# Performance work log

Measured on AMD Instinct MI355X. Metric: run time of the kernel, lower is better.

Reference implementation:

```python
import jax, jax.numpy as jnp
import numpy as np

N = 50000
D_IN = 256
OUT = 16
HEADS = 32
GAT_C = OUT  # out_channels + beta_on(=0)


def _gat_conv(x, src, dst, W, att_src, att_dst, bias):
    """PyG GATConv, concat=False (mean over heads), with self-loops already appended."""
    n = x.shape[0]
    xp = (x @ W).reshape(n, HEADS, GAT_C)            # [N,H,C]
    a_s = jnp.einsum('nhc,hc->nh', xp, att_src)       # [N,H]
    a_d = jnp.einsum('nhc,hc->nh', xp, att_dst)       # [N,H]
    e = jax.nn.leaky_relu(a_s[src] + a_d[dst], 0.2)   # [E,H]
    # segment softmax over incoming edges of each dst node
    m = jax.ops.segment_max(e, dst, num_segments=n)
    e = jnp.exp(e - m[dst])
    s = jax.ops.segment_sum(e, dst, num_segments=n)
    alpha = e / (s[dst] + 1e-16)                      # [E,H]
    out = jax.ops.segment_sum(alpha[:, :, None] * xp[src], dst, num_segments=n)  # [N,H,C]
    return out.mean(axis=1) + bias                    # [N,C]


def setup_inputs() -> dict:
    key = jax.random.key(0)
    ks = jax.random.split(key, 16)
    E = 800000
    x = jax.random.normal(ks[0], (N, D_IN), dtype=jnp.float32)
    edge_index = jax.random.randint(ks[1], (2, E), 0, N, dtype=jnp.int64)
    sc = 1.0 / np.sqrt(D_IN)
    W1 = jax.random.normal(ks[2], (D_IN, HEADS * GAT_C), dtype=jnp.float32) * sc
    att_src1 = jax.random.normal(ks[3], (HEADS, GAT_C), dtype=jnp.float32) * 0.1
    att_dst1 = jax.random.normal(ks[4], (HEADS, GAT_C), dtype=jnp.float32) * 0.1
    b1 = jnp.zeros((GAT_C,), dtype=jnp.float32)
    W2 = jax.random.normal(ks[5], (D_IN, HEADS * GAT_C), dtype=jnp.float32) * sc
    att_src2 = jax.random.normal(ks[6], (HEADS, GAT_C), dtype=jnp.float32) * 0.1
    att_dst2 = jax.random.normal(ks[7], (HEADS, GAT_C), dtype=jnp.float32) * 0.1
    b2 = jnp.zeros((GAT_C,), dtype=jnp.float32)
    lin1_w = jax.random.normal(ks[8], (D_IN, 4 * OUT), dtype=jnp.float32) * sc
    lin1_b = jnp.zeros((4 * OUT,), dtype=jnp.float32)
    lin2_w = jax.random.normal(ks[9], (4 * OUT, OUT), dtype=jnp.float32) * (1.0 / np.sqrt(4 * OUT))
    lin2_b = jnp.zeros((OUT,), dtype=jnp.float32)
    return {"x": x, "edge_index": edge_index,
            "W1": W1, "att_src1": att_src1, "att_dst1": att_dst1, "b1": b1,
            "W2": W2, "att_src2": att_src2, "att_dst2": att_dst2, "b2": b2,
            "lin1_w": lin1_w, "lin1_b": lin1_b, "lin2_w": lin2_w, "lin2_b": lin2_b}


def reference(x, edge_index, W1, att_src1, att_dst1, b1, W2, att_src2, att_dst2, b2,
              lin1_w, lin1_b, lin2_w, lin2_b):
    n = x.shape[0]
    loops = jnp.arange(n, dtype=edge_index.dtype)
    # conv1: flow source_to_target on edge_index -> aggregate src=row0 into dst=row1
    src = jnp.concatenate([edge_index[0], loops])
    dst = jnp.concatenate([edge_index[1], loops])
    x_in = jax.nn.elu(_gat_conv(x, src, dst, W1, att_src1, att_dst1, b1))
    # conv2: flow target_to_source on transposed edge_index -> same effective (src,dst)
    x_out = jax.nn.elu(_gat_conv(x, src, dst, W2, att_src2, att_dst2, b2))
    x1 = jax.nn.elu(x @ lin1_w + lin1_b)
    x_self = jax.nn.elu(x1 @ lin2_w + lin2_b)
    return (x_in, x_out, x_self)
```

## Files before the change

### kernel.cpp

```cpp
#include <hip/hip_runtime.h>

typedef __bf16 bf16x8 __attribute__((ext_vector_type(8)));
typedef float  f32x4  __attribute__((ext_vector_type(4)));
typedef float  f32x2  __attribute__((ext_vector_type(2)));

#define NNODES   50000
#define DIN      256
#define HEADS    32
#define CDIM     16
#define NH       512
#define ERAW     800000
#define SCAN_B   196
#define LDSW     280

__device__ __forceinline__ float b2f(unsigned short u) {
    return __uint_as_float(((unsigned)u) << 16);
}
__device__ __forceinline__ unsigned short f2b(float f) {
    unsigned v = __float_as_uint(f);
    v += 0x7fffu + ((v >> 16) & 1u);
    return (unsigned short)(v >> 16);
}

__global__ void k_detect(const int* __restrict__ ei, int* __restrict__ flag) {
    if (threadIdx.x == 0 && blockIdx.x == 0) {
        int nz = 0;
        #pragma unroll
        for (int t = 0; t < 64; ++t) nz |= ei[2 * t + 1];
        flag[0] = (nz == 0) ? 1 : 0;
    }
}

__global__ void k_zero_deg(int* __restrict__ deg) {
    int i = blockIdx.x * 256 + threadIdx.x;
    if (i < NNODES) deg[i] = 0;
}

__global__ void k_hist(const int* __restrict__ ei, const int* __restrict__ flag,
                       int* __restrict__ deg) {
    int e = blockIdx.x * 256 + threadIdx.x;
    int d = flag[0] ? ei[2 * ERAW + 2 * e] : ei[ERAW + e];
    atomicAdd(&deg[d], 1);
}

__global__ void k_scan_blk(const int* __restrict__ deg, int* __restrict__ part,
                           int* __restrict__ bsum) {
    __shared__ int sm[256];
    int b = blockIdx.x, t = threadIdx.x, i = b * 256 + t;
    int v = (i < NNODES) ? deg[i] : 0;
    sm[t] = v; __syncthreads();
    for (int off = 1; off < 256; off <<= 1) {
        int u = (t >= off) ? sm[t - off] : 0;
        __syncthreads();
        sm[t] += u; __syncthreads();
    }
    if (i < NNODES) part[i] = sm[t] - v;
    if (t == 255) bsum[b] = sm[255];
}

__global__ void k_scan_top(int* __restrict__ bsum) {
    __shared__ int sm[256];
    int t = threadIdx.x;
    int v = (t < SCAN_B) ? bsum[t] : 0;
    sm[t] = v; __syncthreads();
    for (int off = 1; off < 256; off <<= 1) {
        int u = (t >= off) ? sm[t - off] : 0;
        __syncthreads();
        sm[t] += u; __syncthreads();
    }
    if (t < SCAN_B) bsum[t] = sm[t] - v;
}

__global__ void k_scan_add(const int* __restrict__ part, const int* __restrict__ bsum,
                           int* __restrict__ rs, int* __restrict__ cur) {
    int b = blockIdx.x, t = threadIdx.x, i = b * 256 + t;
    if (i < NNODES) { int r = part[i] + bsum[b]; rs[i] = r; cur[i] = r; }
}

__global__ void k_scatter(const int* __restrict__ ei, const int* __restrict__ flag,
                          int* __restrict__ cur, int* __restrict__ csr) {
    int e = blockIdx.x * 256 + threadIdx.x;
    int s, d;
    if (flag[0]) { s = ei[2 * e]; d = ei[2 * ERAW + 2 * e]; }
    else         { s = ei[e];     d = ei[ERAW + e]; }
    int pos = atomicAdd(&cur[d], 1);
    csr[pos] = s;
}

__global__ void k_cast_x(const float* __restrict__ x, unsigned short* __restrict__ xb) {
    int i = blockIdx.x * 256 + threadIdx.x;
    float4 v = *(const float4*)(x + (size_t)i * 4);
    ushort4 o;
    o.x = f2b(v.x); o.y = f2b(v.y); o.z = f2b(v.z); o.w = f2b(v.w);
    *(ushort4*)(xb + (size_t)i * 4) = o;
}

__global__ void k_tr(const float* __restrict__ src, unsigned short* __restrict__ dst,
                     int K, int N) {
    int n = blockIdx.x, k = threadIdx.x;
    dst[n * K + k] = f2b(src[k * N + n]);
}

__global__ void k_tr_gat(const float* __restrict__ src, unsigned short* __restrict__ dst) {
    int n = blockIdx.x, k = threadIdx.x;
    int p = (n & ~63) | (((n & 15) << 2) | ((n >> 4) & 3));
    dst[n * DIN + k] = f2b(src[k * NH + p]);
}

__global__ void __launch_bounds__(256)
k_gemm_xp(const unsigned short* __restrict__ xb,
          const unsigned short* __restrict__ Wt,
          unsigned* __restrict__ xp8) {
    __shared__ unsigned short As[64 * LDSW];
    int row0 = blockIdx.x * 64;
    int tid = threadIdx.x;
    int w = tid >> 6, lane = tid & 63;
    int r = lane & 15, quad = lane >> 4;

    {
        int row = tid >> 2, slot = tid & 3;
        const uint4* g = (const uint4*)(xb + (size_t)(row0 + row) * DIN);
        uint4* l = (uint4*)(As + row * LDSW);
        #pragma unroll
        for (int i = 0; i < 8; ++i)
            l[slot + 4 * i] = g[slot + 4 * i];
    }
    __syncthreads();

    #pragma unroll
    for (int ch = 0; ch < 2; ++ch) {
        f32x4 acc[4][4] = {};
        #pragma unroll
        for (int kc = 0; kc < 8; ++kc) {
            bf16x8 a[4], b[4];
            #pragma unroll
            for (int sub = 0; sub < 4; ++sub)
                a[sub] = *(const bf16x8*)(As + (sub * 16 + r) * LDSW + kc * 32 + quad * 8);
            #pragma unroll
            for (int t = 0; t < 4; ++t) {
                int col = ch * 256 + w * 64 + t * 16 + r;
                b[t] = *(const bf16x8*)(Wt + (size_t)col * DIN + kc * 32 + quad * 8);
            }
            #pragma unroll
            for (int t = 0; t < 4; ++t)
                #pragma unroll
                for (int sub = 0; sub < 4; ++sub)
                    acc[sub][t] = __builtin_amdgcn_mfma_f32_16x16x32_bf16(a[sub], b[t], acc[sub][t], 0, 0, 0);
        }
        #pragma unroll
        for (int sub = 0; sub < 4; ++sub) {
            #pragma unroll
            for (int j = 0; j < 4; ++j) {
                int row = row0 + sub * 16 + quad * 4 + j;
                if (row < NNODES) {
                    unsigned u = (unsigned)__builtin_amdgcn_cvt_pk_fp8_f32(
                                     acc[sub][0][j], acc[sub][1][j], 0, false);
                    u = (unsigned)__builtin_amdgcn_cvt_pk_fp8_f32(
                                     acc[sub][2][j], acc[sub][3][j], (int)u, true);
                    xp8[(size_t)row * 128 + ch * 64 + w * 16 + r] = u;
                }
            }
        }
    }
}

__global__ void k_att(const unsigned* __restrict__ xp8,
                      const float* __restrict__ att_src,
                      const float* __restrict__ att_dst,
                      float* __restrict__ a_s, float* __restrict__ a_d) {
    int tid = threadIdx.x;
    int nd = blockIdx.x * 4 + (tid >> 6);
    int ln = tid & 63;
    int h = ln >> 1;

    const uint2 q = *(const uint2*)(xp8 + (size_t)nd * 128 + ln * 2);
    f32x2 p0 = __builtin_amdgcn_cvt_pk_f32_fp8((int)q.x, false);
    f32x2 p1 = __builtin_amdgcn_cvt_pk_f32_fp8((int)q.x, true);
    f32x2 p2 = __builtin_amdgcn_cvt_pk_f32_fp8((int)q.y, false);
    f32x2 p3 = __builtin_amdgcn_cvt_pk_f32_fp8((int)q.y, true);
    float f[8] = {p0.x, p0.y, p1.x, p1.y, p2.x, p2.y, p3.x, p3.y};

    const f32x4* As4 = (const f32x4*)att_src;
    const f32x4* Ad4 = (const f32x4*)att_dst;
    f32x4 s0 = As4[ln * 2], s1 = As4[ln * 2 + 1];
    f32x4 d0 = Ad4[ln * 2], d1 = Ad4[ln * 2 + 1];

    float ps = f[0]*s0.x + f[1]*s0.y + f[2]*s0.z + f[3]*s0.w
             + f[4]*s1.x + f[5]*s1.y + f[6]*s1.z + f[7]*s1.w;
    float pd = f[0]*d0.x + f[1]*d0.y + f[2]*d0.z + f[3]*d0.w
             + f[4]*d1.x + f[5]*d1.y + f[6]*d1.z + f[7]*d1.w;

    ps += __shfl_xor(ps, 1, 64);
    pd += __shfl_xor(pd, 1, 64);
    if ((ln & 1) == 0) a_s[nd * HEADS + h] = ps;
    else               a_d[nd * HEADS + h] = pd;
}

__global__ void k_conv(const int* __restrict__ csr, const int* __restrict__ rs,
                       const int* __restrict__ deg,
                       const unsigned* __restrict__ xp8,
                       const float* __restrict__ a_s, const float* __restrict__ a_d,
                       const float* __restrict__ bias, float* __restrict__ out) {
    int nd = blockIdx.x * 4 + (threadIdx.x >> 6);
    int ln = threadIdx.x & 63;
    int h  = ln >> 1;
    int cb = (ln & 1) * 8;
    float adn = a_d[nd * HEADS + h];
    int beg = __builtin_amdgcn_readfirstlane(rs[nd]);
    int cnt = __builtin_amdgcn_readfirstlane(deg[nd]);
    const uint2* xv = (const uint2*)xp8;

    float denom = 0.f;
    float acc[8] = {0, 0, 0, 0, 0, 0, 0, 0};

    #define EDGE_BODY(AV, QV)                                              \
    {                                                                      \
        float tt = (AV) + adn;                                             \
        tt = fmaxf(tt, 0.2f * tt);                                         \
        float e = __expf(tt);                                              \
        denom += e;                                                        \
        f32x2 p0 = __builtin_amdgcn_cvt_pk_f32_fp8((int)(QV).x, false);    \
        f32x2 p1 = __builtin_amdgcn_cvt_pk_f32_fp8((int)(QV).x, true);     \
        f32x2 p2 = __builtin_amdgcn_cvt_pk_f32_fp8((int)(QV).y, false);    \
        f32x2 p3 = __builtin_amdgcn_cvt_pk_f32_fp8((int)(QV).y, true);     \
        acc[0] += e * p0.x; acc[1] += e * p0.y;                            \
        acc[2] += e * p1.x; acc[3] += e * p1.y;                            \
        acc[4] += e * p2.x; acc[5] += e * p2.y;                            \
        acc[6] += e * p3.x; acc[7] += e * p3.y;                            \
    }

    {
        float av = a_s[nd * HEADS + h];
        uint2 qv = xv[(size_t)nd * 64 + ln];
        EDGE_BODY(av, qv)
    }

    int i = 0;
    for (; i + 8 <= cnt; i += 8) {
        int sv[8];
        #pragma unroll
        for (int k = 0; k < 8; ++k) sv[k] = csr[beg + i + k];
        float av[8];
        #pragma unroll
        for (int k = 0; k < 8; ++k) av[k] = a_s[sv[k] * HEADS + h];
        uint2 qv[8];
        #pragma unroll
        for (int k = 0; k < 8; ++k) qv[k] = xv[(size_t)sv[k] * 64 + ln];
        #pragma unroll
        for (int k = 0; k < 8; ++k) EDGE_BODY(av[k], qv[k])
    }
    for (; i < cnt; ++i) {
        int s = csr[beg + i];
        float av = a_s[s * HEADS + h];
        uint2 qv = xv[(size_t)s * 64 + ln];
        EDGE_BODY(av, qv)
    }
    #undef EDGE_BODY

    float inv = 1.f / (denom + 1e-16f);
    #pragma unroll
    for (int c = 0; c < 8; ++c) acc[c] *= inv;

    #pragma unroll
    for (int mask = 2; mask <= 32; mask <<= 1) {
        #pragma unroll
        for (int c = 0; c < 8; ++c) acc[c] += __shfl_xor(acc[c], mask, 64);
    }
    if (ln < 2) {
        #pragma unroll
        for (int c2 = 0; c2 < 8; ++c2) {
            int c = cb + c2;
            float o = acc[c2] * (1.0f / HEADS) + bias[c];
            out[(size_t)nd * CDIM + c] = o > 0.f ? o : expm1f(o);
        }
    }
}

__global__ void k_mlp1(const unsigned short* __restrict__ xb,
                       const unsigned short* __restrict__ w1t,
                       const float* __restrict__ bb1, unsigned short* __restrict__ x1) {
    int wave = blockIdx.x * 4 + (threadIdx.x >> 6);
    if (wave >= 782) return;
    int lane = threadIdx.x & 63;
    int r = lane & 15, quad = lane >> 4;
    int row0 = wave * 64;

    f32x4 acc[4][4] = {};
    #pragma unroll
    for (int kc = 0; kc < 8; ++kc) {
        bf16x8 a[4];
        #pragma unroll
        for (int sub = 0; sub < 4; ++sub) {
            int row = row0 + sub * 16 + r;
            if (row0 + sub * 16 < NNODES)
                a[sub] = *(const bf16x8*)(xb + (size_t)row * DIN + kc * 32 + quad * 8);
            else {
                union { unsigned short u[8]; bf16x8 v; } z;
                #pragma unroll
                for (int j = 0; j < 8; ++j) z.u[j] = 0;
                a[sub] = z.v;
            }
        }
        #pragma unroll
        for (int t = 0; t < 4; ++t) {
            int col = t * 16 + r;
            bf16x8 b = *(const bf16x8*)(w1t + (size_t)col * DIN + kc * 32 + quad * 8);
            #pragma unroll
            for (int sub = 0; sub < 4; ++sub)
                acc[sub][t] = __builtin_amdgcn_mfma_f32_16x16x32_bf16(a[sub], b, acc[sub][t], 0, 0, 0);
        }
    }
    #pragma unroll
    for (int sub = 0; sub < 4; ++sub) {
        #pragma unroll
        for (int t = 0; t < 4; ++t) {
            int col = t * 16 + r;
            float bv = bb1[col];
            #pragma unroll
            for (int j = 0; j < 4; ++j) {
                int row = row0 + sub * 16 + quad * 4 + j;
                if (row < NNODES) {
                    float v = acc[sub][t][j] + bv;
                    v = v > 0.f ? v : expm1f(v);
                    x1[(size_t)row * 64 + col] = f2b(v);
                }
            }
        }
    }
}

__global__ void k_mlp2(const unsigned short* __restrict__ x1,
                       const unsigned short* __restrict__ w2t,
                       const float* __restrict__ bb2, float* __restrict__ out) {
    int wave = blockIdx.x * 4 + (threadIdx.x >> 6);
    if (wave >= 3125) return;
    int lane = threadIdx.x & 63;
    int r = lane & 15, quad = lane >> 4;

    f32x4 acc = {};
    #pragma unroll
    for (int kc = 0; kc < 2; ++kc) {
        bf16x8 a = *(const bf16x8*)(x1 + (size_t)(wave * 16 + r) * 64 + kc * 32 + quad * 8);
        bf16x8 b = *(const bf16x8*)(w2t + (size_t)r * 64 + kc * 32 + quad * 8);
        acc = __builtin_amdgcn_mfma_f32_16x16x32_bf16(a, b, acc, 0, 0, 0);
    }
    float bv = bb2[r];
    #pragma unroll
    for (int j = 0; j < 4; ++j) {
        int row = wave * 16 + quad * 4 + j;
        float v = acc[j] + bv;
        v = v > 0.f ? v : expm1f(v);
        out[(size_t)row * CDIM + r] = v;
    }
}

extern "C" void kernel_launch(void* const* d_in, const int* in_sizes, int n_in,
                              void* d_out, int out_size, void* d_ws, size_t ws_size,
                              hipStream_t stream) {
    const float* x  = (const float*)d_in[0];
    const int* ei   = (const int*)d_in[1];
    const float* W[2]    = {(const float*)d_in[2], (const float*)d_in[6]};
    const float* atS[2]  = {(const float*)d_in[3], (const float*)d_in[7]};
    const float* atD[2]  = {(const float*)d_in[4], (const float*)d_in[8]};
    const float* bias[2] = {(const float*)d_in[5], (const float*)d_in[9]};
    const float* w1 = (const float*)d_in[10];
    const float* b1 = (const float*)d_in[11];
    const float* w2 = (const float*)d_in[12];
    const float* b2 = (const float*)d_in[13];
    float* out = (float*)d_out;

    char* ws = (char*)d_ws;
    unsigned* xp8 = (unsigned*)(ws);
    unsigned short* xb  = (unsigned short*)(ws + 25600000);
    unsigned short* Wt  = (unsigned short*)(ws + 51200000);
    unsigned short* w1t = (unsigned short*)(ws + 51462144);
    unsigned short* w2t = (unsigned short*)(ws + 51494912);
    float* a_s = (float*)(ws + 51496960);
    float* a_d = (float*)(ws + 57896960);
    unsigned short* x1 = (unsigned short*)(ws + 51496960);
    int* deg   = (int*)(ws + 64296960);
    int* rs    = (int*)(ws + 64496960);
    int* cur   = (int*)(ws + 64696960);
    int* part  = (int*)(ws + 64896960);
    int* bsum  = (int*)(ws + 65096960);
    int* csr   = (int*)(ws + 65097984);
    int* flag  = (int*)(ws + 68297984);

    k_detect<<<1, 64, 0, stream>>>(ei, flag);
    k_zero_deg<<<SCAN_B, 256, 0, stream>>>(deg);
    k_hist    <<<3125, 256, 0, stream>>>(ei, flag, deg);
    k_scan_blk<<<SCAN_B, 256, 0, stream>>>(deg, part, bsum);
    k_scan_top<<<1, 256, 0, stream>>>(bsum);
    k_scan_add<<<SCAN_B, 256, 0, stream>>>(part, bsum, rs, cur);
    k_scatter <<<3125, 256, 0, stream>>>(ei, flag, cur, csr);

    k_cast_x<<<12500, 256, 0, stream>>>(x, xb);
    k_tr<<<64, 256, 0, stream>>>(w1, w1t, DIN, 64);
    k_tr<<<16, 64, 0, stream>>>(w2, w2t, 64, CDIM);

    for (int cv = 0; cv < 2; ++cv) {
        k_tr_gat <<<512, 256, 0, stream>>>(W[cv], Wt);
        k_gemm_xp<<<782, 256, 0, stream>>>(xb, Wt, xp8);
        k_att    <<<12500, 256, 0, stream>>>(xp8, atS[cv], atD[cv], a_s, a_d);
        k_conv   <<<12500, 256, 0, stream>>>(csr, rs, deg, xp8, a_s, a_d,
                                             bias[cv], out + (size_t)cv * 800000);
    }
    k_mlp1<<<196, 256, 0, stream>>>(xb, w1t, b1, x1);
    k_mlp2<<<782, 256, 0, stream>>>(x1, w2t, b2, out + 1600000);
}
```

Measured before the change: 498.3 us.

## Process two destination nodes per wave in GAT aggregation kernel

Each wavefront in the aggregation kernel now handles two destination nodes, interleaving their neighbor gathers in an unrolled-by-4 loop over the shorter degree. Leftover edges for each node are then handled in separate tails, and the grid is halved. The intent is more independent memory requests in flight per wave and lower per-wave setup and reduction overhead. In exchange it uses more registers, lowers occupancy, and serializes the leftover edges of whichever node has the higher degree.

```diff
diff --git a/kernel.cpp b/kernel.cpp
--- a/kernel.cpp
+++ b/kernel.cpp
@@ -201,77 +201,119 @@
                        const unsigned* __restrict__ xp8,
                        const float* __restrict__ a_s, const float* __restrict__ a_d,
                        const float* __restrict__ bias, float* __restrict__ out) {
-    int nd = blockIdx.x * 4 + (threadIdx.x >> 6);
+    int w  = blockIdx.x * 4 + (threadIdx.x >> 6);
+    int ndA = w * 2, ndB = w * 2 + 1;
     int ln = threadIdx.x & 63;
     int h  = ln >> 1;
     int cb = (ln & 1) * 8;
-    float adn = a_d[nd * HEADS + h];
-    int beg = __builtin_amdgcn_readfirstlane(rs[nd]);
-    int cnt = __builtin_amdgcn_readfirstlane(deg[nd]);
+    float adnA = a_d[ndA * HEADS + h];
+    float adnB = a_d[ndB * HEADS + h];
+    int begA = __builtin_amdgcn_readfirstlane(rs[ndA]);
+    int cntA = __builtin_amdgcn_readfirstlane(deg[ndA]);
+    int begB = __builtin_amdgcn_readfirstlane(rs[ndB]);
+    int cntB = __builtin_amdgcn_readfirstlane(deg[ndB]);
     const uint2* xv = (const uint2*)xp8;
 
-    float denom = 0.f;
-    float acc[8] = {0, 0, 0, 0, 0, 0, 0, 0};
-
-    #define EDGE_BODY(AV, QV)                                              \
+    float denA = 0.f, denB = 0.f;
+    float accA[8] = {0, 0, 0, 0, 0, 0, 0, 0};
+    float accB[8] = {0, 0, 0, 0, 0, 0, 0, 0};
+
+    #define EDGE_BODY(AV, QV, ADN, DEN, ACC)                               \
     {                                                                      \
-        float tt = (AV) + adn;                                             \
+        float tt = (AV) + (ADN);                                           \
         tt = fmaxf(tt, 0.2f * tt);                                         \
         float e = __expf(tt);                                              \
-        denom += e;                                                        \
+        (DEN) += e;                                                        \
         f32x2 p0 = __builtin_amdgcn_cvt_pk_f32_fp8((int)(QV).x, false);    \
         f32x2 p1 = __builtin_amdgcn_cvt_pk_f32_fp8((int)(QV).x, true);     \
         f32x2 p2 = __builtin_amdgcn_cvt_pk_f32_fp8((int)(QV).y, false);    \
         f32x2 p3 = __builtin_amdgcn_cvt_pk_f32_fp8((int)(QV).y, true);     \
-        acc[0] += e * p0.x; acc[1] += e * p0.y;                            \
-        acc[2] += e * p1.x; acc[3] += e * p1.y;                            \
-        acc[4] += e * p2.x; acc[5] += e * p2.y;                            \
-        acc[6] += e * p3.x; acc[7] += e * p3.y;                            \
+        (ACC)[0] += e * p0.x; (ACC)[1] += e * p0.y;                        \
+        (ACC)[2] += e * p1.x; (ACC)[3] += e * p1.y;                        \
+        (ACC)[4] += e * p2.x; (ACC)[5] += e * p2.y;                        \
+        (ACC)[6] += e * p3.x; (ACC)[7] += e * p3.y;                        \
     }
 
     {
-        float av = a_s[nd * HEADS + h];
-        uint2 qv = xv[(size_t)nd * 64 + ln];
-        EDGE_BODY(av, qv)
-    }
-
+        float avA = a_s[ndA * HEADS + h];
+        float avB = a_s[ndB * HEADS + h];
+        uint2 qvA = xv[(size_t)ndA * 64 + ln];
+        uint2 qvB = xv[(size_t)ndB * 64 + ln];
+        EDGE_BODY(avA, qvA, adnA, denA, accA)
+        EDGE_BODY(avB, qvB, adnB, denB, accB)
+    }
+
+    int mn = cntA < cntB ? cntA : cntB;
     int i = 0;
-    for (; i + 8 <= cnt; i += 8) {
-        int sv[8];
-        #pragma unroll
-        for (int k = 0; k < 8; ++k) sv[k] = csr[beg + i + k];
-        float av[8];
-        #pragma unroll
-        for (int k = 0; k < 8; ++k) av[k] = a_s[sv[k] * HEADS + h];
-        uint2 qv[8];
-        #pragma unroll
-        for (int k = 0; k < 8; ++k) qv[k] = xv[(size_t)sv[k] * 64 + ln];
-        #pragma unroll
-        for (int k = 0; k < 8; ++k) EDGE_BODY(av[k], qv[k])
-    }
-    for (; i < cnt; ++i) {
-        int s = csr[beg + i];
+    for (; i + 4 <= mn; i += 4) {
+        int svA[4], svB[4];
+        #pragma unroll
+        for (int k = 0; k < 4; ++k) svA[k] = csr[begA + i + k];
+        #pragma unroll
+        for (int k = 0; k < 4; ++k) svB[k] = csr[begB + i + k];
+        float avA[4], avB[4];
+        #pragma unroll
+        for (int k = 0; k < 4; ++k) avA[k] = a_s[svA[k] * HEADS + h];
+        #pragma unroll
+        for (int k = 0; k < 4; ++k) avB[k] = a_s[svB[k] * HEADS + h];
+        uint2 qvA[4], qvB[4];
+        #pragma unroll
+        for (int k = 0; k < 4; ++k) qvA[k] = xv[(size_t)svA[k] * 64 + ln];
+        #pragma unroll
+        for (int k = 0; k < 4; ++k) qvB[k] = xv[(size_t)svB[k] * 64 + ln];
+        #pragma unroll
+        for (int k = 0; k < 4; ++k) {
+            EDGE_BODY(avA[k], qvA[k], adnA, denA, accA)
+            EDGE_BODY(avB[k], qvB[k], adnB, denB, accB)
+        }
+    }
+    for (; i < mn; ++i) {
+        int sA = csr[begA + i], sB = csr[begB + i];
+        float avA = a_s[sA * HEADS + h], avB = a_s[sB * HEADS + h];
+        uint2 qvA = xv[(size_t)sA * 64 + ln], qvB = xv[(size_t)sB * 64 + ln];
+        EDGE_BODY(avA, qvA, adnA, denA, accA)
+        EDGE_BODY(avB, qvB, adnB, denB, accB)
+    }
+    for (int j = i; j < cntA; ++j) {
+        int s = csr[begA + j];
         float av = a_s[s * HEADS + h];
         uint2 qv = xv[(size_t)s * 64 + ln];
-        EDGE_BODY(av, qv)
+        EDGE_BODY(av, qv, adnA, denA, accA)
+    }
+    for (int j = i; j < cntB; ++j) {
+        int s = csr[begB + j];
+        float av = a_s[s * HEADS + h];
+        uint2 qv = xv[(size_t)s * 64 + ln];
+        EDGE_BODY(av, qv, adnB, denB, accB)
     }
     #undef EDGE_BODY
 
-    float inv = 1.f / (denom + 1e-16f);
-    #pragma unroll
-    for (int c = 0; c < 8; ++c) acc[c] *= inv;
+    float invA = 1.f / (denA + 1e-16f);
+    float invB = 1.f / (denB + 1e-16f);
+    #pragma unroll
+    for (int c = 0; c < 8; ++c) { accA[c] *= invA; accB[c] *= invB; }
 
     #pragma unroll
     for (int mask = 2; mask <= 32; mask <<= 1) {
         #pragma unroll
-        for (int c = 0; c < 8; ++c) acc[c] += __shfl_xor(acc[c], mask, 64);
+        for (int c = 0; c < 8; ++c) {
+            accA[c] += __shfl_xor(accA[c], mask, 64);
+            accB[c] += __shfl_xor(accB[c], mask, 64);
+        }
     }
     if (ln < 2) {
         #pragma unroll
         for (int c2 = 0; c2 < 8; ++c2) {
             int c = cb + c2;
-            float o = acc[c2] * (1.0f / HEADS) + bias[c];
-            out[(size_t)nd * CDIM + c] = o > 0.f ? o : expm1f(o);
+            float o = accA[c2] * (1.0f / HEADS) + bias[c];
+            out[(size_t)ndA * CDIM + c] = o > 0.f ? o : expm1f(o);
+        }
+    } else if (ln < 4) {
+        #pragma unroll
+        for (int c2 = 0; c2 < 8; ++c2) {
+            int c = cb + c2;
+            float o = accB[c2] * (1.0f / HEADS) + bias[c];
+            out[(size_t)ndB * CDIM + c] = o > 0.f ? o : expm1f(o);
         }
     }
 }
@@ -402,8 +444,8 @@
         k_tr_gat <<<512, 256, 0, stream>>>(W[cv], Wt);
         k_gemm_xp<<<782, 256, 0, stream>>>(xb, Wt, xp8);
         k_att    <<<12500, 256, 0, stream>>>(xp8, atS[cv], atD[cv], a_s, a_d);
-        k_conv   <<<12500, 256, 0, stream>>>(csr, rs, deg, xp8, a_s, a_d,
-                                             bias[cv], out + (size_t)cv * 800000);
+        k_conv   <<<6250, 256, 0, stream>>>(csr, rs, deg, xp8, a_s, a_d,
+                                            bias[cv], out + (size_t)cv * 800000);
     }
     k_mlp1<<<196, 256, 0, stream>>>(xb, w1t, b1, x1);
     k_mlp2<<<782, 256, 0, stream>>>(x1, w2t, b2, out + 1600000);
```

Measured after the change: 512.8 us. +2.9%, slower.

## Software-pipeline edge gathers in GAT conv and use exp2 with prescaled logits

Applied to the files above, without the earlier changes.

Restructures the per-node edge loop into a software pipeline over groups of four edges. The next group's CSR indices are prefetched and the current group's gathers are issued before the previous group is computed, with sched_barrier keeping the order. The tail is handled by clamping indices and masking contributions to zero, not by a scalar remainder loop. Attention logits are prescaled by log2(e) in the projection kernel so the conv can use the hardware exp2, which saves a multiply per edge. The cost is more live registers and redundant loads for padded tail edges.

```diff
diff --git a/kernel.cpp b/kernel.cpp
--- a/kernel.cpp
+++ b/kernel.cpp
@@ -12,6 +12,12 @@
 #define ERAW     800000
 #define SCAN_B   196
 #define LDSW     280
+
+#if __has_builtin(__builtin_amdgcn_exp2f)
+#define EXP2(x) __builtin_amdgcn_exp2f(x)
+#else
+#define EXP2(x) __expf((x) * 0.6931471805599453f)
+#endif
 
 __device__ __forceinline__ float b2f(unsigned short u) {
     return __uint_as_float(((unsigned)u) << 16);
@@ -192,8 +198,9 @@
 
     ps += __shfl_xor(ps, 1, 64);
     pd += __shfl_xor(pd, 1, 64);
-    if ((ln & 1) == 0) a_s[nd * HEADS + h] = ps;
-    else               a_d[nd * HEADS + h] = pd;
+    const float LOG2E = 1.4426950408889634f;
+    if ((ln & 1) == 0) a_s[nd * HEADS + h] = ps * LOG2E;
+    else               a_d[nd * HEADS + h] = pd * LOG2E;
 }
 
 __global__ void k_conv(const int* __restrict__ csr, const int* __restrict__ rs,
@@ -213,11 +220,12 @@
     float denom = 0.f;
     float acc[8] = {0, 0, 0, 0, 0, 0, 0, 0};
 
-    #define EDGE_BODY(AV, QV)                                              \
+    #define EDGE_BODY(AV, QV, LIVE)                                        \
     {                                                                      \
         float tt = (AV) + adn;                                             \
         tt = fmaxf(tt, 0.2f * tt);                                         \
-        float e = __expf(tt);                                              \
+        float e = EXP2(tt);                                                \
+        e = (LIVE) ? e : 0.f;                                              \
         denom += e;                                                        \
         f32x2 p0 = __builtin_amdgcn_cvt_pk_f32_fp8((int)(QV).x, false);    \
         f32x2 p1 = __builtin_amdgcn_cvt_pk_f32_fp8((int)(QV).x, true);     \
@@ -229,31 +237,57 @@
         acc[6] += e * p3.x; acc[7] += e * p3.y;                            \
     }
 
-    {
-        float av = a_s[nd * HEADS + h];
-        uint2 qv = xv[(size_t)nd * 64 + ln];
-        EDGE_BODY(av, qv)
-    }
-
-    int i = 0;
-    for (; i + 8 <= cnt; i += 8) {
-        int sv[8];
-        #pragma unroll
-        for (int k = 0; k < 8; ++k) sv[k] = csr[beg + i + k];
-        float av[8];
-        #pragma unroll
-        for (int k = 0; k < 8; ++k) av[k] = a_s[sv[k] * HEADS + h];
-        uint2 qv[8];
-        #pragma unroll
-        for (int k = 0; k < 8; ++k) qv[k] = xv[(size_t)sv[k] * 64 + ln];
-        #pragma unroll
-        for (int k = 0; k < 8; ++k) EDGE_BODY(av[k], qv[k])
-    }
-    for (; i < cnt; ++i) {
-        int s = csr[beg + i];
-        float av = a_s[s * HEADS + h];
-        uint2 qv = xv[(size_t)s * 64 + ln];
-        EDGE_BODY(av, qv)
+    float avS = a_s[nd * HEADS + h];
+    uint2 qvS = xv[(size_t)nd * 64 + ln];
+    int nb = (cnt + 3) >> 2;
+    float avP[4]; uint2 qvP[4]; int svN[4];
+    if (nb > 0) {
+        #pragma unroll
+        for (int k = 0; k < 4; ++k) {
+            int ce = k < cnt ? k : cnt - 1;
+            int s = csr[beg + ce];
+            avP[k] = a_s[s * HEADS + h];
+            qvP[k] = xv[(size_t)s * 64 + ln];
+        }
+        #pragma unroll
+        for (int k = 0; k < 4; ++k) {
+            int idx = 4 + k;
+            int ce = idx < cnt ? idx : cnt - 1;
+            svN[k] = csr[beg + ce];
+        }
+    }
+    __builtin_amdgcn_sched_barrier(0);
+    EDGE_BODY(avS, qvS, 1)
+
+    for (int b = 1; b < nb; ++b) {
+        float avN[4]; uint2 qvN[4];
+        #pragma unroll
+        for (int k = 0; k < 4; ++k) {
+            int s = svN[k];
+            avN[k] = a_s[s * HEADS + h];
+            qvN[k] = xv[(size_t)s * 64 + ln];
+        }
+        {
+            int nbase = (b + 1 < nb ? b + 1 : nb - 1) * 4;
+            #pragma unroll
+            for (int k = 0; k < 4; ++k) {
+                int idx = nbase + k;
+                int ce = idx < cnt ? idx : cnt - 1;
+                svN[k] = csr[beg + ce];
+            }
+        }
+        __builtin_amdgcn_sched_barrier(0);
+        #pragma unroll
+        for (int k = 0; k < 4; ++k) EDGE_BODY(avP[k], qvP[k], 1)
+        #pragma unroll
+        for (int k = 0; k < 4; ++k) { avP[k] = avN[k]; qvP[k] = qvN[k]; }
+    }
+    if (nb > 0) {
+        #pragma unroll
+        for (int k = 0; k < 4; ++k) {
+            int idx = (nb - 1) * 4 + k;
+            EDGE_BODY(avP[k], qvP[k], idx < cnt)
+        }
     }
     #undef EDGE_BODY
 
```

New measurement: 494.2 us. No clear change (-0.8%).
